# Kernel tuning notes

Hardware: AMD Instinct MI355X
Metric: run time of the kernel (lower is better)

The kernel has to match this reference:

```python
import jax, jax.numpy as jnp
import numpy as np

NUM_HIDDEN = 1024
NUM_ATTN = 16
HEAD_DIM = NUM_HIDDEN // NUM_ATTN


def setup_inputs() -> dict:
    key = jax.random.key(0)
    ks = jax.random.split(key, 9)
    B, Sq, Sk = 4, 2048, 2048
    query = jax.random.normal(ks[0], (B, Sq, 1), dtype=jnp.float32)
    k_in = jax.random.normal(ks[1], (B, Sk, 1), dtype=jnp.float32)
    value = jax.random.normal(ks[2], (B, Sk, NUM_HIDDEN), dtype=jnp.float32)
    s1 = 1.0  # fan_in=1 for query/key projections
    sv = 1.0 / np.sqrt(NUM_HIDDEN)
    Wq = jax.random.uniform(ks[3], (1, NUM_HIDDEN), jnp.float32, -s1, s1)
    bq = jax.random.uniform(ks[4], (NUM_HIDDEN,), jnp.float32, -s1, s1)
    Wk = jax.random.uniform(ks[5], (1, NUM_HIDDEN), jnp.float32, -s1, s1)
    bk = jax.random.uniform(ks[6], (NUM_HIDDEN,), jnp.float32, -s1, s1)
    Wv = jax.random.uniform(ks[7], (NUM_HIDDEN, NUM_HIDDEN), jnp.float32, -sv, sv)
    bv = jax.random.uniform(ks[8], (NUM_HIDDEN,), jnp.float32, -sv, sv)
    return {"query": query, "key": k_in, "value": value,
            "Wq": Wq, "bq": bq, "Wk": Wk, "bk": bk, "Wv": Wv, "bv": bv}


def reference(query, key, value, Wq, bq, Wk, bk, Wv, bv):
    B, Sq, _ = query.shape
    Sk = key.shape[1]
    H, D = NUM_ATTN, HEAD_DIM
    # linear projections (dropout is identity in eval mode)
    q = (query @ Wq + bq).reshape(B, Sq, H, D)
    k = (key @ Wk + bk).reshape(B, Sk, H, D)
    v = (value @ Wv + bv).reshape(B, Sk, H, D)
    # permute(2,0,1,3).view(h*b, s, d)
    q = q.transpose(2, 0, 1, 3).reshape(H * B, Sq, D)
    k = k.transpose(2, 0, 1, 3).reshape(H * B, Sk, D)
    v = v.transpose(2, 0, 1, 3).reshape(H * B, Sk, D)
    attn = jnp.einsum('nqd,nkd->nqk', q, k) / jnp.sqrt(jnp.float32(D))
    attn = jax.nn.softmax(attn, axis=-1)
    return jnp.einsum('nqk,nkd->nqd', attn, v)
```

## Files before the change

kernel.cpp:

```cpp
#include <hip/hip_runtime.h>
#include <cstdint>


#define WS_P   1024
#define WS_PW  197632
#define WS_CZ  394240

__global__ __launch_bounds__(256) void k_prep(const float* __restrict__ key,
                                              const float* __restrict__ Wq,
                                              const float* __restrict__ bq,
                                              const float* __restrict__ Wk,
                                              float* __restrict__ ws) {
  __shared__ float kxl[2048];
  __shared__ float wmax[4];
  __shared__ float wz[4][48];
  int t = threadIdx.x, l = t & 63, w = t >> 6;
  int b = blockIdx.x;
  float m = 0.f;
  for (int j = t; j < 2048; j += 256) {
    float v = key[b * 2048 + j];
    kxl[j] = v;
    m = fmaxf(m, fabsf(v));
  }
  for (int off = 32; off; off >>= 1) m = fmaxf(m, __shfl_xor(m, off));
  if (l == 0) wmax[w] = m;
  __syncthreads();
  float S = fmaxf(fmaxf(wmax[0], wmax[1]), fmaxf(wmax[2], wmax[3]));
  if (t == 0) ws[b] = S;
  float rs = 1.0f / S;

  float z[48];
#pragma unroll
  for (int q = 0; q < 48; ++q) z[q] = 0.f;
  for (int jj = 0; jj < 8; ++jj) {
    float kh = kxl[t * 8 + jj] * rs;
    float p = 1.f;
#pragma unroll
    for (int q = 0; q < 48; ++q) { z[q] += p; p *= kh; }
  }
#pragma unroll
  for (int q = 0; q < 48; ++q) {
    float v = z[q];
    for (int off = 32; off; off >>= 1) v += __shfl_xor(v, off);
    if (l == 0) wz[w][q] = v;
  }
  __syncthreads();
  if (t < 48) ws[64 + b * 48 + t] = wz[0][t] + wz[1][t] + wz[2][t] + wz[3][t];

  if (b == 0 && t < 32) {
    int h = t & 15; bool isB = t >= 16;
    float a = 0.f;
    for (int d = 0; d < 64; ++d)
      a = fmaf(isB ? bq[h * 64 + d] : Wq[h * 64 + d], Wk[h * 64 + d], a);
    ws[4 + (isB ? 16 : 0) + h] = a;
  }
}

__global__ __launch_bounds__(256) void k_mom(const float* __restrict__ value,
                                             const float* __restrict__ key,
                                             const float* __restrict__ ws,
                                             float* __restrict__ part) {
  __shared__ float khl[64];
  int tid = threadIdx.x;
  int ct = blockIdx.x, jc = blockIdx.y, b = blockIdx.z;
  int c = ct * 256 + tid;
  float rs = 1.0f / ws[b];
  if (tid < 64) khl[tid] = key[b * 2048 + jc * 64 + tid] * rs;
  __syncthreads();

  float acc[48];
#pragma unroll
  for (int q = 0; q < 48; ++q) acc[q] = 0.f;
  const float* vp = value + ((size_t)(b * 2048 + jc * 64) << 10) + c;
  for (int j4 = 0; j4 < 64; j4 += 4) {
    float v0 = vp[(size_t)(j4 + 0) << 10];
    float v1 = vp[(size_t)(j4 + 1) << 10];
    float v2 = vp[(size_t)(j4 + 2) << 10];
    float v3 = vp[(size_t)(j4 + 3) << 10];
#pragma unroll
    for (int u = 0; u < 4; ++u) {
      float v = (u == 0) ? v0 : (u == 1) ? v1 : (u == 2) ? v2 : v3;
      float kh = khl[j4 + u];
      float k2 = kh * kh;
      float q0 = 1.f, q1 = kh, q2 = k2, q3 = k2 * kh;
      float k4 = k2 * k2;
#pragma unroll
      for (int g = 0; g < 12; ++g) {
        acc[4 * g + 0] = fmaf(q0, v, acc[4 * g + 0]);
        acc[4 * g + 1] = fmaf(q1, v, acc[4 * g + 1]);
        acc[4 * g + 2] = fmaf(q2, v, acc[4 * g + 2]);
        acc[4 * g + 3] = fmaf(q3, v, acc[4 * g + 3]);
        q0 *= k4; q1 *= k4; q2 *= k4; q3 *= k4;
      }
    }
  }
  size_t base = ((size_t)((b * 32 + jc) * 48) << 10) + c;
#pragma unroll
  for (int q = 0; q < 48; ++q) part[base + ((size_t)q << 10)] = acc[q];
}

__global__ __launch_bounds__(256) void k_red(const float* __restrict__ part,
                                             float* __restrict__ ws) {
  int gid = blockIdx.x * 256 + threadIdx.x;
  int c = gid & 1023; int bt = gid >> 10; int t = bt % 48; int b = bt / 48;
  float s = 0.f;
  for (int jc = 0; jc < 32; ++jc)
    s += part[((size_t)((b * 32 + jc) * 48 + t) << 10) + c];
  ws[WS_P + ((size_t)(b * 48 + t) << 10) + c] = s;
}

__global__ __launch_bounds__(256) void k_proj(const float* __restrict__ ws,
                                              const float* __restrict__ Wv,
                                              float* __restrict__ pp) {
  __shared__ float Pl[16 * 64];
  int tid = threadIdx.x;
  int cc = blockIdx.x, hdt = blockIdx.y;
  int b = blockIdx.z & 3, tt = blockIdx.z >> 2;
  int hd = hdt * 256 + tid;
  for (int x = tid; x < 16 * 64; x += 256) {
    int q = x >> 6, cl = x & 63;
    Pl[x] = ws[WS_P + ((size_t)(b * 48 + tt * 16 + q) << 10) + cc * 64 + cl];
  }
  __syncthreads();
  float acc[16];
#pragma unroll
  for (int q = 0; q < 16; ++q) acc[q] = 0.f;
  for (int c = 0; c < 64; ++c) {
    float wv = Wv[((size_t)(cc * 64 + c) << 10) + hd];
#pragma unroll
    for (int q = 0; q < 16; ++q)
      acc[q] = fmaf(Pl[(q << 6) + c], wv, acc[q]);
  }
  size_t base = ((size_t)((cc * 4 + b) * 48 + tt * 16) << 10) + hd;
#pragma unroll
  for (int q = 0; q < 16; ++q) pp[base + ((size_t)q << 10)] = acc[q];
}

__global__ __launch_bounds__(256) void k_projred(const float* __restrict__ pp,
                                                 float* __restrict__ ws) {
  int gid = blockIdx.x * 256 + threadIdx.x;
  int hd = gid & 1023; int bt = gid >> 10; int t = bt % 48; int b = bt / 48;
  float s = 0.f;
  for (int cc = 0; cc < 16; ++cc)
    s += pp[((size_t)((cc * 4 + b) * 48 + t) << 10) + hd];
  ws[WS_PW + ((size_t)(b * 48 + t) << 10) + hd] = s;
}

__global__ __launch_bounds__(256) void k_z(const float* __restrict__ query,
                                           float* __restrict__ ws) {
  int bid = blockIdx.x;
  int h = bid >> 5; int b = (bid >> 3) & 3; int it = bid & 7;
  int i = it * 256 + threadIdx.x;
  float S = ws[b];
  float Ah = ws[4 + h], Bkh = ws[20 + h];
  float qx = query[b * 2048 + i];
  float cp = fmaf(Ah, qx, Bkh) * 0.125f * S;
  const float* zc = ws + 64 + b * 48;
  float r = zc[47];
#pragma unroll
  for (int t = 47; t >= 1; --t)
    r = fmaf(cp * (1.0f / (float)t), r, zc[t - 1]);
  float rz = 1.0f / r;
  size_t o = ((size_t)((h * 4 + b) * 2048 + i)) * 2;
  ws[WS_CZ + o] = cp;
  ws[WS_CZ + o + 1] = rz;
}

__global__ __launch_bounds__(256) void k_out(const float* __restrict__ ws,
                                             const float* __restrict__ bv,
                                             float* __restrict__ out) {
  int tid = threadIdx.x; int l = tid & 63; int w = tid >> 6;
  int qt = blockIdx.x, b = blockIdx.y, h = blockIdx.z;
  float a[48];
  const float* PW = ws + WS_PW + ((size_t)(b * 48) << 10) + h * 64 + l;
#pragma unroll
  for (int q = 0; q < 48; ++q) a[q] = PW[(size_t)q << 10];
  float bvd = bv[h * 64 + l];
  const float* cz = ws + WS_CZ + ((size_t)((h * 4 + b) * 2048 + qt * 256 + w * 64)) * 2;
  size_t ob = (((size_t)((h * 4 + b) * 2048) + qt * 256 + w * 64) << 6) + l;
  for (int r = 0; r < 64; ++r) {
    float cp = cz[r * 2], rz = cz[r * 2 + 1];
    float acc = a[47];
#pragma unroll
    for (int t = 47; t >= 1; --t)
      acc = fmaf(cp * (1.0f / (float)t), acc, a[t - 1]);
    out[ob + ((size_t)r << 6)] = fmaf(acc, rz, bvd);
  }
}

extern "C" void kernel_launch(void* const* d_in, const int* in_sizes, int n_in,
                              void* d_out, int out_size, void* d_ws, size_t ws_size,
                              hipStream_t stream) {
  const float* query = (const float*)d_in[0];
  const float* key   = (const float*)d_in[1];
  const float* value = (const float*)d_in[2];
  const float* Wq    = (const float*)d_in[3];
  const float* bq    = (const float*)d_in[4];
  const float* Wk    = (const float*)d_in[5];
  const float* Wv    = (const float*)d_in[7];
  const float* bv    = (const float*)d_in[8];
  float* out = (float*)d_out;
  float* ws  = (float*)d_ws;
  float* stage = (float*)d_out;

  k_prep<<<dim3(4), 256, 0, stream>>>(key, Wq, bq, Wk, ws);
  k_mom<<<dim3(4, 32, 4), 256, 0, stream>>>(value, key, ws, stage);
  k_red<<<dim3(768), 256, 0, stream>>>(stage, ws);
  k_proj<<<dim3(16, 4, 12), 256, 0, stream>>>(ws, Wv, stage);
  k_projred<<<dim3(768), 256, 0, stream>>>(stage, ws);
  k_z<<<dim3(512), 256, 0, stream>>>(query, ws);
  k_out<<<dim3(8, 4, 16), 256, 0, stream>>>(ws, bv, out);
}
```

Before: 183.9 us.

## Split moment kernel into finer key chunks staged through LDS with three passes

The moment-accumulation kernel now covers 32 keys per block instead of 64, doubling the grid, and first stages the value tile into shared memory with float4 loads. It computes the 48 power moments in three 16-wide passes, using precomputed kh^16 and kh^32 bases, which cuts the live accumulator registers from 48 to 16 per pass. Partial sums and projection partials move from the output buffer to dedicated workspace regions, so the reduction now reads twice as many partials. Every kernel also gets a launch-bounds minimum of one block, which lets the compiler use more registers at the cost of occupancy.

New measurement: 197.0 us. 7.1% more time.

```diff
diff --git a/kernel.cpp b/kernel.cpp
--- a/kernel.cpp
+++ b/kernel.cpp
@@ -2,15 +2,18 @@
 #include <cstdint>
 
 
-#define WS_P   1024
-#define WS_PW  197632
-#define WS_CZ  394240
-
-__global__ __launch_bounds__(256) void k_prep(const float* __restrict__ key,
-                                              const float* __restrict__ Wq,
-                                              const float* __restrict__ bq,
-                                              const float* __restrict__ Wk,
-                                              float* __restrict__ ws) {
+#define WS_P    1024
+#define WS_PW   197632
+#define WS_CZ   394240
+#define WS_PART 1048576
+#define WS_PP   14680064
+#define MOM_JC  32
+
+__global__ __launch_bounds__(256, 1) void k_prep(const float* __restrict__ key,
+                                                 const float* __restrict__ Wq,
+                                                 const float* __restrict__ bq,
+                                                 const float* __restrict__ Wk,
+                                                 float* __restrict__ ws) {
   __shared__ float kxl[2048];
   __shared__ float wmax[4];
   __shared__ float wz[4][48];
@@ -56,62 +59,84 @@
   }
 }
 
-__global__ __launch_bounds__(256) void k_mom(const float* __restrict__ value,
-                                             const float* __restrict__ key,
-                                             const float* __restrict__ ws,
-                                             float* __restrict__ part) {
-  __shared__ float khl[64];
+__global__ __launch_bounds__(256, 1) void k_mom(const float* __restrict__ value,
+                                                const float* __restrict__ key,
+                                                const float* __restrict__ ws,
+                                                float* __restrict__ wsout) {
+  __shared__ float tile[MOM_JC * 256];
+  __shared__ float khl[MOM_JC];
+  __shared__ float khb[2 * MOM_JC];
   int tid = threadIdx.x;
   int ct = blockIdx.x, jc = blockIdx.y, b = blockIdx.z;
-  int c = ct * 256 + tid;
+  int c0 = ct * 256, j0 = jc * MOM_JC;
   float rs = 1.0f / ws[b];
-  if (tid < 64) khl[tid] = key[b * 2048 + jc * 64 + tid] * rs;
-  __syncthreads();
-
-  float acc[48];
-#pragma unroll
-  for (int q = 0; q < 48; ++q) acc[q] = 0.f;
-  const float* vp = value + ((size_t)(b * 2048 + jc * 64) << 10) + c;
-  for (int j4 = 0; j4 < 64; j4 += 4) {
-    float v0 = vp[(size_t)(j4 + 0) << 10];
-    float v1 = vp[(size_t)(j4 + 1) << 10];
-    float v2 = vp[(size_t)(j4 + 2) << 10];
-    float v3 = vp[(size_t)(j4 + 3) << 10];
-#pragma unroll
-    for (int u = 0; u < 4; ++u) {
-      float v = (u == 0) ? v0 : (u == 1) ? v1 : (u == 2) ? v2 : v3;
-      float kh = khl[j4 + u];
-      float k2 = kh * kh;
-      float q0 = 1.f, q1 = kh, q2 = k2, q3 = k2 * kh;
-      float k4 = k2 * k2;
-#pragma unroll
-      for (int g = 0; g < 12; ++g) {
-        acc[4 * g + 0] = fmaf(q0, v, acc[4 * g + 0]);
-        acc[4 * g + 1] = fmaf(q1, v, acc[4 * g + 1]);
-        acc[4 * g + 2] = fmaf(q2, v, acc[4 * g + 2]);
-        acc[4 * g + 3] = fmaf(q3, v, acc[4 * g + 3]);
-        q0 *= k4; q1 *= k4; q2 *= k4; q3 *= k4;
+  if (tid < MOM_JC) {
+    float kh = key[b * 2048 + j0 + tid] * rs;
+    khl[tid] = kh;
+    float kh2 = kh * kh, kh4 = kh2 * kh2, kh8 = kh4 * kh4;
+    float kh16 = kh8 * kh8;
+    khb[tid] = kh16;
+    khb[MOM_JC + tid] = kh16 * kh16;
+  }
+  {
+    const float* vsrc = value + (((size_t)(b * 2048 + j0)) << 10) + c0;
+    int x = tid * 4;
+#pragma unroll
+    for (int p = 0; p < (MOM_JC * 256) / 1024; ++p) {
+      int idx = p * 1024 + x;
+      int row = idx >> 8, col = idx & 255;
+      *reinterpret_cast<float4*>(&tile[idx]) =
+          *reinterpret_cast<const float4*>(&vsrc[((size_t)row << 10) + col]);
+    }
+  }
+  __syncthreads();
+
+  size_t pb0 = WS_PART + (((size_t)((b * 64 + jc) * 48)) << 10) + c0 + tid;
+#pragma unroll
+  for (int tc = 0; tc < 3; ++tc) {
+    float acc[16];
+#pragma unroll
+    for (int a = 0; a < 16; ++a) acc[a] = 0.f;
+    for (int j = 0; j < MOM_JC; j += 4) {
+      float4 khq = *reinterpret_cast<const float4*>(&khl[j]);
+      float4 bq4 = (tc == 0) ? make_float4(1.f, 1.f, 1.f, 1.f)
+                             : *reinterpret_cast<const float4*>(&khb[(tc - 1) * MOM_JC + j]);
+#pragma unroll
+      for (int u = 0; u < 4; ++u) {
+        float v = tile[(j + u) * 256 + tid];
+        float kh = reinterpret_cast<const float*>(&khq)[u];
+        float base = reinterpret_cast<const float*>(&bq4)[u];
+        float kh2 = kh * kh;
+        float k4 = kh2 * kh2;
+        float q0 = base, q1 = base * kh, q2 = base * kh2, q3 = q2 * kh;
+#pragma unroll
+        for (int g = 0; g < 4; ++g) {
+          acc[4 * g + 0] = fmaf(q0, v, acc[4 * g + 0]);
+          acc[4 * g + 1] = fmaf(q1, v, acc[4 * g + 1]);
+          acc[4 * g + 2] = fmaf(q2, v, acc[4 * g + 2]);
+          acc[4 * g + 3] = fmaf(q3, v, acc[4 * g + 3]);
+          if (g < 3) { q0 *= k4; q1 *= k4; q2 *= k4; q3 *= k4; }
+        }
       }
     }
-  }
-  size_t base = ((size_t)((b * 32 + jc) * 48) << 10) + c;
-#pragma unroll
-  for (int q = 0; q < 48; ++q) part[base + ((size_t)q << 10)] = acc[q];
-}
-
-__global__ __launch_bounds__(256) void k_red(const float* __restrict__ part,
-                                             float* __restrict__ ws) {
+#pragma unroll
+    for (int a = 0; a < 16; ++a)
+      wsout[pb0 + (((size_t)(tc * 16 + a)) << 10)] = acc[a];
+  }
+}
+
+__global__ __launch_bounds__(256, 1) void k_red(float* __restrict__ ws) {
   int gid = blockIdx.x * 256 + threadIdx.x;
   int c = gid & 1023; int bt = gid >> 10; int t = bt % 48; int b = bt / 48;
   float s = 0.f;
-  for (int jc = 0; jc < 32; ++jc)
-    s += part[((size_t)((b * 32 + jc) * 48 + t) << 10) + c];
-  ws[WS_P + ((size_t)(b * 48 + t) << 10) + c] = s;
-}
-
-__global__ __launch_bounds__(256) void k_proj(const float* __restrict__ ws,
-                                              const float* __restrict__ Wv,
-                                              float* __restrict__ pp) {
+  for (int jc = 0; jc < 64; ++jc)
+    s += ws[WS_PART + (((size_t)((b * 64 + jc) * 48 + t)) << 10) + c];
+  ws[WS_P + (((size_t)(b * 48 + t)) << 10) + c] = s;
+}
+
+__global__ __launch_bounds__(256, 1) void k_proj(const float* __restrict__ wsin,
+                                                 const float* __restrict__ Wv,
+                                                 float* __restrict__ ws) {
   __shared__ float Pl[16 * 64];
   int tid = threadIdx.x;
   int cc = blockIdx.x, hdt = blockIdx.y;
@@ -119,35 +144,34 @@
   int hd = hdt * 256 + tid;
   for (int x = tid; x < 16 * 64; x += 256) {
     int q = x >> 6, cl = x & 63;
-    Pl[x] = ws[WS_P + ((size_t)(b * 48 + tt * 16 + q) << 10) + cc * 64 + cl];
+    Pl[x] = wsin[WS_P + (((size_t)(b * 48 + tt * 16 + q)) << 10) + cc * 64 + cl];
   }
   __syncthreads();
   float acc[16];
 #pragma unroll
   for (int q = 0; q < 16; ++q) acc[q] = 0.f;
   for (int c = 0; c < 64; ++c) {
-    float wv = Wv[((size_t)(cc * 64 + c) << 10) + hd];
+    float wv = Wv[(((size_t)(cc * 64 + c)) << 10) + hd];
 #pragma unroll
     for (int q = 0; q < 16; ++q)
       acc[q] = fmaf(Pl[(q << 6) + c], wv, acc[q]);
   }
-  size_t base = ((size_t)((cc * 4 + b) * 48 + tt * 16) << 10) + hd;
-#pragma unroll
-  for (int q = 0; q < 16; ++q) pp[base + ((size_t)q << 10)] = acc[q];
-}
-
-__global__ __launch_bounds__(256) void k_projred(const float* __restrict__ pp,
-                                                 float* __restrict__ ws) {
+  size_t base = WS_PP + (((size_t)((cc * 4 + b) * 48 + tt * 16)) << 10) + hd;
+#pragma unroll
+  for (int q = 0; q < 16; ++q) ws[base + (((size_t)q) << 10)] = acc[q];
+}
+
+__global__ __launch_bounds__(256, 1) void k_projred(float* __restrict__ ws) {
   int gid = blockIdx.x * 256 + threadIdx.x;
   int hd = gid & 1023; int bt = gid >> 10; int t = bt % 48; int b = bt / 48;
   float s = 0.f;
   for (int cc = 0; cc < 16; ++cc)
-    s += pp[((size_t)((cc * 4 + b) * 48 + t) << 10) + hd];
-  ws[WS_PW + ((size_t)(b * 48 + t) << 10) + hd] = s;
-}
-
-__global__ __launch_bounds__(256) void k_z(const float* __restrict__ query,
-                                           float* __restrict__ ws) {
+    s += ws[WS_PP + (((size_t)((cc * 4 + b) * 48 + t)) << 10) + hd];
+  ws[WS_PW + (((size_t)(b * 48 + t)) << 10) + hd] = s;
+}
+
+__global__ __launch_bounds__(256, 1) void k_z(const float* __restrict__ query,
+                                              float* __restrict__ ws) {
   int bid = blockIdx.x;
   int h = bid >> 5; int b = (bid >> 3) & 3; int it = bid & 7;
   int i = it * 256 + threadIdx.x;
@@ -166,25 +190,25 @@
   ws[WS_CZ + o + 1] = rz;
 }
 
-__global__ __launch_bounds__(256) void k_out(const float* __restrict__ ws,
-                                             const float* __restrict__ bv,
-                                             float* __restrict__ out) {
+__global__ __launch_bounds__(256, 1) void k_out(const float* __restrict__ ws,
+                                                const float* __restrict__ bv,
+                                                float* __restrict__ out) {
   int tid = threadIdx.x; int l = tid & 63; int w = tid >> 6;
   int qt = blockIdx.x, b = blockIdx.y, h = blockIdx.z;
   float a[48];
-  const float* PW = ws + WS_PW + ((size_t)(b * 48) << 10) + h * 64 + l;
-#pragma unroll
-  for (int q = 0; q < 48; ++q) a[q] = PW[(size_t)q << 10];
+  const float* PW = ws + WS_PW + (((size_t)(b * 48)) << 10) + h * 64 + l;
+#pragma unroll
+  for (int q = 0; q < 48; ++q) a[q] = PW[((size_t)q) << 10];
   float bvd = bv[h * 64 + l];
   const float* cz = ws + WS_CZ + ((size_t)((h * 4 + b) * 2048 + qt * 256 + w * 64)) * 2;
-  size_t ob = (((size_t)((h * 4 + b) * 2048) + qt * 256 + w * 64) << 6) + l;
+  size_t ob = ((((size_t)((h * 4 + b) * 2048)) + qt * 256 + w * 64) << 6) + l;
   for (int r = 0; r < 64; ++r) {
     float cp = cz[r * 2], rz = cz[r * 2 + 1];
     float acc = a[47];
 #pragma unroll
     for (int t = 47; t >= 1; --t)
       acc = fmaf(cp * (1.0f / (float)t), acc, a[t - 1]);
-    out[ob + ((size_t)r << 6)] = fmaf(acc, rz, bvd);
+    out[ob + (((size_t)r) << 6)] = fmaf(acc, rz, bvd);
   }
 }
 
@@ -201,13 +225,12 @@
   const float* bv    = (const float*)d_in[8];
   float* out = (float*)d_out;
   float* ws  = (float*)d_ws;
-  float* stage = (float*)d_out;
 
   k_prep<<<dim3(4), 256, 0, stream>>>(key, Wq, bq, Wk, ws);
-  k_mom<<<dim3(4, 32, 4), 256, 0, stream>>>(value, key, ws, stage);
-  k_red<<<dim3(768), 256, 0, stream>>>(stage, ws);
-  k_proj<<<dim3(16, 4, 12), 256, 0, stream>>>(ws, Wv, stage);
-  k_projred<<<dim3(768), 256, 0, stream>>>(stage, ws);
+  k_mom<<<dim3(4, 64, 4), 256, 0, stream>>>(value, key, ws, ws);
+  k_red<<<dim3(768), 256, 0, stream>>>(ws);
+  k_proj<<<dim3(16, 4, 12), 256, 0, stream>>>(ws, Wv, ws);
+  k_projred<<<dim3(768), 256, 0, stream>>>(ws);
   k_z<<<dim3(512), 256, 0, stream>>>(query, ws);
   k_out<<<dim3(8, 4, 16), 256, 0, stream>>>(ws, bv, out);
 }
```
